# Kernel tuning notes

Hardware: AMD Instinct MI355X
Metric: run time of the kernel (lower is better)

Reference implementation:

```python
import jax, jax.numpy as jnp
from jax import lax
import numpy as np


def gru_last(seq, Wih, Whh, bih, bhh):
    """Run a torch-style GRU over seq [N, T, C] and return only h_T [N, H].

    Gate order matches torch.nn.GRU: (r, z, n);
    n = tanh(W_in x + b_in + r * (W_hn h + b_hn)).
    """
    N = seq.shape[0]
    H = Whh.shape[1]

    def step(h, x_t):
        gi = x_t @ Wih.T + bih          # [N, 3H]
        gh = h @ Whh.T + bhh            # [N, 3H]
        i_r, i_z, i_n = jnp.split(gi, 3, axis=-1)
        h_r, h_z, h_n = jnp.split(gh, 3, axis=-1)
        r = jax.nn.sigmoid(i_r + h_r)
        z = jax.nn.sigmoid(i_z + h_z)
        n = jnp.tanh(i_n + r * h_n)
        h_new = (1.0 - z) * n + z * h
        return h_new, None

    h0 = jnp.zeros((N, H), dtype=seq.dtype)
    hT, _ = lax.scan(step, h0, jnp.swapaxes(seq, 0, 1))  # scan over T
    return hT


def setup_inputs() -> dict:
    key = jax.random.key(0)
    ks = jax.random.split(key, 12)
    B, C, T, Fq, H = 8, 64, 256, 256, 128
    s = 0.05
    return {
        "x": jax.random.normal(ks[0], (B, C, T, Fq), dtype=jnp.float32),
        "Wih_t": jax.random.normal(ks[1], (3 * H, C), dtype=jnp.float32) * s,
        "Whh_t": jax.random.normal(ks[2], (3 * H, H), dtype=jnp.float32) * s,
        "bih_t": jax.random.normal(ks[3], (3 * H,), dtype=jnp.float32) * s,
        "bhh_t": jax.random.normal(ks[4], (3 * H,), dtype=jnp.float32) * s,
        "Wih_f": jax.random.normal(ks[5], (3 * H, C), dtype=jnp.float32) * s,
        "Whh_f": jax.random.normal(ks[6], (3 * H, H), dtype=jnp.float32) * s,
        "bih_f": jax.random.normal(ks[7], (3 * H,), dtype=jnp.float32) * s,
        "bhh_f": jax.random.normal(ks[8], (3 * H,), dtype=jnp.float32) * s,
        "Wp": jax.random.normal(ks[9], (C, H), dtype=jnp.float32) * s,
        "bp": jax.random.normal(ks[10], (C,), dtype=jnp.float32) * s,
    }


def reference(x, Wih_t, Whh_t, bih_t, bhh_t, Wih_f, Whh_f, bih_f, bhh_f, Wp, bp):
    B, C, T, Fq = x.shape
    H = Whh_t.shape[1]

    # time GRU: sequences of length T, one per (batch, freq)
    t_in = jnp.transpose(x, (0, 3, 2, 1)).reshape(B * Fq, T, C)
    h_t = gru_last(t_in, Wih_t, Whh_t, bih_t, bhh_t)          # [B*F, H]
    t_vec = jnp.transpose(h_t.reshape(B, Fq, H), (0, 2, 1))    # [B, H, F]

    # freq GRU: sequences of length F, one per (batch, time)
    f_in = jnp.transpose(x, (0, 2, 3, 1)).reshape(B * T, Fq, C)
    h_f = gru_last(f_in, Wih_f, Whh_f, bih_f, bhh_f)          # [B*T, H]
    f_vec = jnp.transpose(h_f.reshape(B, T, H), (0, 2, 1))    # [B, H, T]

    # t_feat [B,H,F,1] expanded along dim2 to T (requires F == T),
    # f_feat [B,H,T,1] expanded along dim3 to F; fused is constant along F.
    s = t_vec + f_vec                                          # [B, H, T]  (F == T)
    out_t = jnp.einsum("ch,bht->bct", Wp, s) + bp[None, :, None]  # 1x1 conv
    return jnp.broadcast_to(out_t[:, :, :, None], (B, C, T, Fq))
```

## Files before the change

kernel.cpp:

```cpp
#include <hip/hip_runtime.h>

#define B_ 8
#define C_ 64
#define T_ 256
#define F_ 256
#define H_ 128
#define TF_ (T_*F_)

typedef _Float16 half_t;
typedef _Float16 half8 __attribute__((ext_vector_type(8)));
typedef float float4v __attribute__((ext_vector_type(4)));

#if __has_builtin(__builtin_amdgcn_exp2f)
#define EXP2F(x) __builtin_amdgcn_exp2f(x)
#else
static __device__ inline float EXP2F(float x) { float r; asm("v_exp_f32 %0, %1" : "=v"(r) : "v"(x)); return r; }
#endif
#if __has_builtin(__builtin_amdgcn_rcpf)
#define RCPF(x) __builtin_amdgcn_rcpf(x)
#else
static __device__ inline float RCPF(float x) { float r; asm("v_rcp_f32 %0, %1" : "=v"(r) : "v"(x)); return r; }
#endif

#define NEG_L2E  (-1.4426950408889634f)
#define NEG_2L2E (-2.8853900817779268f)

__global__ __launch_bounds__(256) void k_transpose(const float* __restrict__ x,
                                                   half_t* __restrict__ xt) {
    __shared__ float lds[64 * 65];
    int blk = blockIdx.x;
    int b   = blk >> 10;
    int tf0 = (blk & 1023) << 6;
    int tid = threadIdx.x;
    int tfl   = tid & 63;
    int cbase = tid >> 6;
    const float* xp = x + (size_t)(b * C_) * TF_ + tf0 + tfl;
#pragma unroll
    for (int i = 0; i < 16; ++i) {
        int c = cbase + i * 4;
        lds[tfl * 65 + c] = xp[(size_t)c * TF_];
    }
    __syncthreads();
    int row = tid >> 2;
    int c0  = (tid & 3) << 4;
    float v[16];
#pragma unroll
    for (int k = 0; k < 16; ++k) v[k] = lds[row * 65 + c0 + k];
    half8 o0, o1;
#pragma unroll
    for (int k = 0; k < 8; ++k) { o0[k] = (half_t)v[k]; o1[k] = (half_t)v[8 + k]; }
    half_t* op = xt + ((size_t)b * TF_ + tf0 + row) * C_ + c0;
    *(half8*)op       = o0;
    *(half8*)(op + 8) = o1;
}

__device__ inline half8 load_w8s(const float* __restrict__ p, float s) {
    half8 r;
#pragma unroll
    for (int k = 0; k < 8; ++k) r[k] = (half_t)(p[k] * s);
    return r;
}

#define MFMA(a, b, c) __builtin_amdgcn_mfma_f32_16x16x32_f16((a), (b), (c), 0, 0, 0)

__global__ __launch_bounds__(512, 2) void k_gru(
    const half_t* __restrict__ xt,
    const float* __restrict__ Wih_t, const float* __restrict__ Whh_t,
    const float* __restrict__ bih_t, const float* __restrict__ bhh_t,
    const float* __restrict__ Wih_f, const float* __restrict__ Whh_f,
    const float* __restrict__ bih_f, const float* __restrict__ bhh_f,
    float* __restrict__ h_t_out, float* __restrict__ h_f_out) {
    __shared__ half_t hbuf0[16 * 136];
    __shared__ half_t hbuf1[16 * 136];

    int tid  = threadIdx.x;
    int w    = tid >> 6;
    int lane = tid & 63;
    int nidx = lane & 15;
    int quad = lane >> 4;

    int bi  = blockIdx.x;
    bool isf = bi >= 128;
    int lbi = bi & 127;
    int b   = lbi >> 4;
    int g16 = (lbi & 15) << 4;

    const float* Wih = isf ? Wih_f : Wih_t;
    const float* Whh = isf ? Whh_f : Whh_t;
    const float* bih = isf ? bih_f : bih_t;
    const float* bhh = isf ? bhh_f : bhh_t;
    float* hout      = isf ? h_f_out : h_t_out;

    size_t Sm = isf ? (size_t)(F_ * C_) : (size_t)C_;
    size_t Ss = isf ? (size_t)C_ : (size_t)(F_ * C_);
    size_t abase = (size_t)b * TF_ * C_ + (size_t)g16 * Sm;

    int gr = w * 16 + nidx;
    int gz = gr + 128;
    int gn = gr + 256;
    int ko = quad * 8;

    half8 wir0 = load_w8s(Wih + gr * 64 + ko,      NEG_L2E);
    half8 wir1 = load_w8s(Wih + gr * 64 + 32 + ko, NEG_L2E);
    half8 wiz0 = load_w8s(Wih + gz * 64 + ko,      NEG_L2E);
    half8 wiz1 = load_w8s(Wih + gz * 64 + 32 + ko, NEG_L2E);
    half8 win0 = load_w8s(Wih + gn * 64 + ko,      NEG_2L2E);
    half8 win1 = load_w8s(Wih + gn * 64 + 32 + ko, NEG_2L2E);
    half8 whr[4], whz[4], whn[4];
#pragma unroll
    for (int kt = 0; kt < 4; ++kt) {
        whr[kt] = load_w8s(Whh + gr * 128 + kt * 32 + ko, NEG_L2E);
        whz[kt] = load_w8s(Whh + gz * 128 + kt * 32 + ko, NEG_L2E);
        whn[kt] = load_w8s(Whh + gn * 128 + kt * 32 + ko, NEG_2L2E);
    }
    float br  = NEG_L2E  * (bih[gr] + bhh[gr]);
    float bz  = NEG_L2E  * (bih[gz] + bhh[gz]);
    float bin = NEG_2L2E * bih[gn];
    float bhn = NEG_2L2E * bhh[gn];

    for (int idx = tid; idx < 16 * 136; idx += 512) hbuf0[idx] = (half_t)0.f;
    float h_old[4] = {0.f, 0.f, 0.f, 0.f};
    __syncthreads();

    const half_t* ap = xt + abase + (size_t)nidx * Sm + ko;
    half8 xaA0 = *(const half8*)ap;
    half8 xaA1 = *(const half8*)(ap + 32);
    ap += Ss;
    half8 xaB0, xaB1;

#define GRU_STEP(XA0, XA1, RBUF, WBUF)                                          \
    {                                                                           \
        const half_t* hrow = (RBUF) + nidx * 136 + ko;                          \
        half8 ha0 = *(const half8*)(hrow);                                      \
        half8 ha1 = *(const half8*)(hrow + 32);                                 \
        half8 ha2 = *(const half8*)(hrow + 64);                                 \
        half8 ha3 = *(const half8*)(hrow + 96);                                 \
        float4v ar  = {br, br, br, br};                                         \
        float4v az  = {bz, bz, bz, bz};                                         \
        float4v ain = {bin, bin, bin, bin};                                     \
        float4v ahn = {bhn, bhn, bhn, bhn};                                     \
        ar  = MFMA(XA0, wir0, ar);  ar  = MFMA(XA1, wir1, ar);                  \
        az  = MFMA(XA0, wiz0, az);  az  = MFMA(XA1, wiz1, az);                  \
        ain = MFMA(XA0, win0, ain); ain = MFMA(XA1, win1, ain);                 \
        ar  = MFMA(ha0, whr[0], ar);  ar  = MFMA(ha1, whr[1], ar);              \
        ar  = MFMA(ha2, whr[2], ar);  ar  = MFMA(ha3, whr[3], ar);              \
        az  = MFMA(ha0, whz[0], az);  az  = MFMA(ha1, whz[1], az);              \
        az  = MFMA(ha2, whz[2], az);  az  = MFMA(ha3, whz[3], az);              \
        ahn = MFMA(ha0, whn[0], ahn); ahn = MFMA(ha1, whn[1], ahn);             \
        ahn = MFMA(ha2, whn[2], ahn); ahn = MFMA(ha3, whn[3], ahn);             \
        _Pragma("unroll")                                                       \
        for (int rg = 0; rg < 4; ++rg) {                                        \
            float r  = RCPF(1.f + EXP2F(ar[rg]));                               \
            float z  = RCPF(1.f + EXP2F(az[rg]));                               \
            float np = ain[rg] + r * ahn[rg];           \
            float n  = 2.f * RCPF(1.f + EXP2F(np)) - 1.f;                       \
            float h  = n + z * (h_old[rg] - n);                                 \
            h_old[rg] = h;                                                      \
            (WBUF)[(quad * 4 + rg) * 136 + w * 16 + nidx] = (half_t)h;          \
        }                                                                       \
        __syncthreads();                                                        \
    }

    for (int it = 0; it < 128; ++it) {
        xaB0 = *(const half8*)ap;
        xaB1 = *(const half8*)(ap + 32);
        ap += Ss;
        GRU_STEP(xaA0, xaA1, hbuf0, hbuf1)
        xaA0 = *(const half8*)ap;
        xaA1 = *(const half8*)(ap + 32);
        ap += Ss;
        GRU_STEP(xaB0, xaB1, hbuf1, hbuf0)
    }
#undef GRU_STEP

    int srow = (b << 8) + g16;
#pragma unroll
    for (int rg = 0; rg < 4; ++rg) {
        hout[(size_t)(srow + quad * 4 + rg) * H_ + w * 16 + nidx] = h_old[rg];
    }
}

__global__ __launch_bounds__(256) void k_out(const float* __restrict__ h_t,
                                             const float* __restrict__ h_f,
                                             const float* __restrict__ Wp,
                                             const float* __restrict__ bp,
                                             float* __restrict__ out) {
    __shared__ float sv[128];
    __shared__ float part[4][64];
    __shared__ float orow[64];
    int blk = blockIdx.x;
    int b = blk >> 8;
    int i = blk & 255;
    int tid = threadIdx.x;
    size_t hoff = ((size_t)(b * 256 + i)) * 128;
    if (tid < 128) sv[tid] = h_t[hoff + tid] + h_f[hoff + tid];
    __syncthreads();
    int c = tid & 63;
    int q = tid >> 6;
    float p = 0.f;
    const float* wp = Wp + c * 128 + q * 32;
#pragma unroll
    for (int k = 0; k < 32; ++k) p += wp[k] * sv[q * 32 + k];
    part[q][c] = p;
    __syncthreads();
    if (tid < 64) orow[tid] = part[0][tid] + part[1][tid] + part[2][tid] + part[3][tid] + bp[tid];
    __syncthreads();
    int wv   = tid >> 6;
    int lane = tid & 63;
#pragma unroll
    for (int itr = 0; itr < 16; ++itr) {
        int cc = itr * 4 + wv;
        float v = orow[cc];
        float4v vv = {v, v, v, v};
        *(float4v*)(out + (((size_t)(b * 64 + cc)) * 256 + i) * 256 + lane * 4) = vv;
    }
}

extern "C" void kernel_launch(void* const* d_in, const int* in_sizes, int n_in,
                              void* d_out, int out_size, void* d_ws, size_t ws_size,
                              hipStream_t stream) {
    const float* x     = (const float*)d_in[0];
    const float* Wih_t = (const float*)d_in[1];
    const float* Whh_t = (const float*)d_in[2];
    const float* bih_t = (const float*)d_in[3];
    const float* bhh_t = (const float*)d_in[4];
    const float* Wih_f = (const float*)d_in[5];
    const float* Whh_f = (const float*)d_in[6];
    const float* bih_f = (const float*)d_in[7];
    const float* bhh_f = (const float*)d_in[8];
    const float* Wp    = (const float*)d_in[9];
    const float* bp    = (const float*)d_in[10];
    float* out = (float*)d_out;

    half_t* xt     = (half_t*)d_out;
    float* h_t_out = (float*)((char*)d_ws);
    float* h_f_out = (float*)((char*)d_ws + (size_t)2048 * 128 * 4);

    k_transpose<<<8192, 256, 0, stream>>>(x, xt);
    k_gru<<<256, 512, 0, stream>>>(xt, Wih_t, Whh_t, bih_t, bhh_t,
                                   Wih_f, Whh_f, bih_f, bhh_f, h_t_out, h_f_out);
    k_out<<<2048, 256, 0, stream>>>(h_t_out, h_f_out, Wp, bp, out);
}
```

Baseline: 455.2 us.

## Precompute next-step input projection off critical path and split recurrent MFMA chains

Moves the input-projection MFMAs for the next timestep to after the gate computation, so they overlap with the barrier instead of sitting on the dependent recurrent chain. Splits each recurrent gate accumulation into two independent MFMA chains to shorten dependency latency. Also vectorises the transpose kernel's global loads to float4. The last iteration reads input one step past the sequence end, a possible out-of-bounds read, and register pressure rises.

Measured after the change: 436.1 us. -4.2%, faster.

```diff
diff --git a/kernel.cpp b/kernel.cpp
--- a/kernel.cpp
+++ b/kernel.cpp
@@ -32,13 +32,15 @@
     int b   = blk >> 10;
     int tf0 = (blk & 1023) << 6;
     int tid = threadIdx.x;
-    int tfl   = tid & 63;
-    int cbase = tid >> 6;
-    const float* xp = x + (size_t)(b * C_) * TF_ + tf0 + tfl;
-#pragma unroll
-    for (int i = 0; i < 16; ++i) {
-        int c = cbase + i * 4;
-        lds[tfl * 65 + c] = xp[(size_t)c * TF_];
+    int s = tid & 15;
+    int q = tid >> 4;
+    const float* xp = x + (size_t)(b * C_) * TF_ + tf0 + s * 4;
+#pragma unroll
+    for (int i = 0; i < 4; ++i) {
+        int c = q + i * 16;
+        float4v v = *(const float4v*)(xp + (size_t)c * TF_);
+#pragma unroll
+        for (int j = 0; j < 4; ++j) lds[(s * 4 + j) * 65 + c] = v[j];
     }
     __syncthreads();
     int row = tid >> 2;
@@ -120,56 +122,66 @@
 
     for (int idx = tid; idx < 16 * 136; idx += 512) hbuf0[idx] = (half_t)0.f;
     float h_old[4] = {0.f, 0.f, 0.f, 0.f};
-    __syncthreads();
 
     const half_t* ap = xt + abase + (size_t)nidx * Sm + ko;
-    half8 xaA0 = *(const half8*)ap;
-    half8 xaA1 = *(const half8*)(ap + 32);
+    half8 xA0 = *(const half8*)ap;
+    half8 xA1 = *(const half8*)(ap + 32);
     ap += Ss;
-    half8 xaB0, xaB1;
-
-#define GRU_STEP(XA0, XA1, RBUF, WBUF)                                          \
+    half8 xB0 = *(const half8*)ap;
+    half8 xB1 = *(const half8*)(ap + 32);
+    ap += Ss;
+
+    float4v xr = {br, br, br, br};
+    float4v xz = {bz, bz, bz, bz};
+    float4v xn = {bin, bin, bin, bin};
+    xr = MFMA(xA0, wir0, xr); xr = MFMA(xA1, wir1, xr);
+    xz = MFMA(xA0, wiz0, xz); xz = MFMA(xA1, wiz1, xz);
+    xn = MFMA(xA0, win0, xn); xn = MFMA(xA1, win1, xn);
+    __syncthreads();
+
+#define GRU_STEP(RBUF, WBUF, XC0, XC1, XP0, XP1)                                \
     {                                                                           \
         const half_t* hrow = (RBUF) + nidx * 136 + ko;                          \
         half8 ha0 = *(const half8*)(hrow);                                      \
         half8 ha1 = *(const half8*)(hrow + 32);                                 \
         half8 ha2 = *(const half8*)(hrow + 64);                                 \
         half8 ha3 = *(const half8*)(hrow + 96);                                 \
-        float4v ar  = {br, br, br, br};                                         \
-        float4v az  = {bz, bz, bz, bz};                                         \
-        float4v ain = {bin, bin, bin, bin};                                     \
-        float4v ahn = {bhn, bhn, bhn, bhn};                                     \
-        ar  = MFMA(XA0, wir0, ar);  ar  = MFMA(XA1, wir1, ar);                  \
-        az  = MFMA(XA0, wiz0, az);  az  = MFMA(XA1, wiz1, az);                  \
-        ain = MFMA(XA0, win0, ain); ain = MFMA(XA1, win1, ain);                 \
-        ar  = MFMA(ha0, whr[0], ar);  ar  = MFMA(ha1, whr[1], ar);              \
-        ar  = MFMA(ha2, whr[2], ar);  ar  = MFMA(ha3, whr[3], ar);              \
-        az  = MFMA(ha0, whz[0], az);  az  = MFMA(ha1, whz[1], az);              \
-        az  = MFMA(ha2, whz[2], az);  az  = MFMA(ha3, whz[3], az);              \
-        ahn = MFMA(ha0, whn[0], ahn); ahn = MFMA(ha1, whn[1], ahn);             \
-        ahn = MFMA(ha2, whn[2], ahn); ahn = MFMA(ha3, whn[3], ahn);             \
+        XP0 = *(const half8*)ap;                                                \
+        XP1 = *(const half8*)(ap + 32);                                         \
+        ap += Ss;                                                               \
+        float4v hr  = {0.f, 0.f, 0.f, 0.f};                                     \
+        float4v hz  = {0.f, 0.f, 0.f, 0.f};                                     \
+        float4v hna = {bhn, bhn, bhn, bhn};                                     \
+        float4v hnb = {0.f, 0.f, 0.f, 0.f};                                     \
+        xr  = MFMA(ha0, whr[0], xr);  xr  = MFMA(ha1, whr[1], xr);              \
+        hr  = MFMA(ha2, whr[2], hr);  hr  = MFMA(ha3, whr[3], hr);              \
+        xz  = MFMA(ha0, whz[0], xz);  xz  = MFMA(ha1, whz[1], xz);              \
+        hz  = MFMA(ha2, whz[2], hz);  hz  = MFMA(ha3, whz[3], hz);              \
+        hna = MFMA(ha0, whn[0], hna); hna = MFMA(ha1, whn[1], hna);             \
+        hnb = MFMA(ha2, whn[2], hnb); hnb = MFMA(ha3, whn[3], hnb);             \
         _Pragma("unroll")                                                       \
         for (int rg = 0; rg < 4; ++rg) {                                        \
-            float r  = RCPF(1.f + EXP2F(ar[rg]));                               \
-            float z  = RCPF(1.f + EXP2F(az[rg]));                               \
-            float np = ain[rg] + r * ahn[rg];           \
+            float r  = RCPF(1.f + EXP2F(xr[rg] + hr[rg]));                      \
+            float z  = RCPF(1.f + EXP2F(xz[rg] + hz[rg]));                      \
+            float np = xn[rg] + r * (hna[rg] + hnb[rg]);                        \
             float n  = 2.f * RCPF(1.f + EXP2F(np)) - 1.f;                       \
             float h  = n + z * (h_old[rg] - n);                                 \
             h_old[rg] = h;                                                      \
             (WBUF)[(quad * 4 + rg) * 136 + w * 16 + nidx] = (half_t)h;          \
         }                                                                       \
+              \
+        xr[0] = br;  xr[1] = br;  xr[2] = br;  xr[3] = br;                      \
+        xz[0] = bz;  xz[1] = bz;  xz[2] = bz;  xz[3] = bz;                      \
+        xn[0] = bin; xn[1] = bin; xn[2] = bin; xn[3] = bin;                     \
+        xr = MFMA(XC0, wir0, xr); xr = MFMA(XC1, wir1, xr);                     \
+        xz = MFMA(XC0, wiz0, xz); xz = MFMA(XC1, wiz1, xz);                     \
+        xn = MFMA(XC0, win0, xn); xn = MFMA(XC1, win1, xn);                     \
         __syncthreads();                                                        \
     }
 
     for (int it = 0; it < 128; ++it) {
-        xaB0 = *(const half8*)ap;
-        xaB1 = *(const half8*)(ap + 32);
-        ap += Ss;
-        GRU_STEP(xaA0, xaA1, hbuf0, hbuf1)
-        xaA0 = *(const half8*)ap;
-        xaA1 = *(const half8*)(ap + 32);
-        ap += Ss;
-        GRU_STEP(xaB0, xaB1, hbuf1, hbuf0)
+        GRU_STEP(hbuf0, hbuf1, xB0, xB1, xA0, xA1)
+        GRU_STEP(hbuf1, hbuf0, xA0, xA1, xB0, xB1)
     }
 #undef GRU_STEP
 
```
